# Optimization experiments

Measured on AMD Instinct MI355X. Metric: run time of the kernel, lower is better.

The kernel has to match this reference:

```python
import jax, jax.numpy as jnp
import numpy as np

# Expert output sizes per answer type: yes/no, number, other (VQA v2)
SIZES = [2, 482, 3129]
MAX_ANS = max(SIZES)  # 3129, padded output width
D_IN = 1024
D_HID = 1000
BATCH = 16384
N_TYPES = len(SIZES)


def setup_inputs() -> dict:
    key = jax.random.key(0)
    ks = jax.random.split(key, 2 + 4 * N_TYPES)
    inp = {
        "hidden_states": jax.random.normal(ks[0], (BATCH, D_IN), dtype=jnp.float32),
        "question_type_output": jax.random.normal(ks[1], (BATCH, N_TYPES), dtype=jnp.float32),
    }
    # Learned params for each expert MLP: Linear(1024->1000), Tanh, Linear(1000->n_e)
    for e, n_out in enumerate(SIZES):
        k1, k2, k3, k4 = ks[2 + 4 * e], ks[3 + 4 * e], ks[4 + 4 * e], ks[5 + 4 * e]
        inp[f"w1_{e}"] = jax.random.normal(k1, (D_IN, D_HID), dtype=jnp.float32) * 0.02
        inp[f"b1_{e}"] = jax.random.normal(k2, (D_HID,), dtype=jnp.float32) * 0.02
        inp[f"w2_{e}"] = jax.random.normal(k3, (D_HID, n_out), dtype=jnp.float32) * 0.02
        inp[f"b2_{e}"] = jax.random.normal(k4, (n_out,), dtype=jnp.float32) * 0.02
    return inp


def _expert(x, w1, b1, w2, b2):
    # Linear -> Dropout(eval: identity) -> Tanh -> Linear
    return jnp.tanh(x @ w1 + b1) @ w2 + b2


def reference(hidden_states, question_type_output,
              w1_0, b1_0, w2_0, b2_0,
              w1_1, b1_1, w2_1, b2_1,
              w1_2, b1_2, w2_2, b2_2):
    params = [(w1_0, b1_0, w2_0, b2_0),
              (w1_1, b1_1, w2_1, b2_1),
              (w1_2, b1_2, w2_2, b2_2)]
    # Route each sample to the expert of its argmax question type.
    pred = jnp.argmax(question_type_output, axis=1)  # [B] int
    out = jnp.zeros((hidden_states.shape[0], MAX_ANS), dtype=hidden_states.dtype)
    # Small fixed loop over N_TYPES experts (structurally distinct weights);
    # each expert runs batched over all samples, then a mask selects routed rows.
    for e, (w1, b1, w2, b2) in enumerate(params):
        o = _expert(hidden_states, w1, b1, w2, b2)          # [B, n_e]
        o = jnp.pad(o, ((0, 0), (0, MAX_ANS - o.shape[1])))  # zero-pad to [B, MAX]
        out = jnp.where((pred == e)[:, None], o, out)
    return out
```

## Files before the change

### kernel.cpp

```cpp
#include <hip/hip_runtime.h>

typedef __attribute__((ext_vector_type(8))) __bf16 bf16x8;
typedef __attribute__((ext_vector_type(4))) float f32x4;

constexpr int BATCH = 16384;
constexpr int DIN   = 1024;
constexpr int DHID  = 1000;
constexpr int MAXA  = 3129;
constexpr int MBMAX = 131;

constexpr size_t SZ_AP  = (size_t)MBMAX * 32 * 8192;
constexpr size_t SZ_HP  = SZ_AP;
constexpr size_t SZ_W1P = 3 * 8 * 32 * 8192;
constexpr size_t SZ_W2P = 30 * 32 * 8192;
constexpr size_t WS_HP  = 0;
constexpr size_t WS_W1P = WS_HP + SZ_HP;
constexpr size_t WS_W2P = WS_W1P + SZ_W1P;
constexpr size_t WS_CNT = WS_W2P + SZ_W2P;
constexpr size_t WS_IDX = WS_CNT + 64;
constexpr size_t WS_AP  = WS_IDX + 3 * BATCH * 4;
constexpr size_t WS_NEED = WS_AP + SZ_AP;

constexpr int PA_BLK = 2096;
constexpr int PW1_BLK = 1536;
constexpr int PW2_BLK = 1920;

__device__ __forceinline__ ushort f2bf(float f) {
    return __builtin_bit_cast(ushort, (__bf16)f);
}

__device__ __forceinline__ void gload16(const void* g, void* l) {
    __builtin_amdgcn_global_load_lds((const __attribute__((address_space(1))) void*)g,
                                     (__attribute__((address_space(3))) void*)l, 16, 0, 0);
}

__global__ void route_k(const float* __restrict__ qt, int* __restrict__ counts,
                        int* __restrict__ idx) {
    int i = blockIdx.x * 256 + threadIdx.x;
    if (i >= BATCH) return;
    float a = qt[3 * i], b = qt[3 * i + 1], c = qt[3 * i + 2];
    int p = 0; float m = a;
    if (b > m) { m = b; p = 1; }
    if (c > m) { m = c; p = 2; }
    int pos = atomicAdd(&counts[p], 1);
    idx[p * BATCH + pos] = i;
}

__global__ void pack_all_k(const float* __restrict__ hs,
                           const float* __restrict__ w1_0, const float* __restrict__ w1_1,
                           const float* __restrict__ w1_2,
                           const float* __restrict__ w2_0, const float* __restrict__ w2_1,
                           const float* __restrict__ w2_2,
                           const int* __restrict__ counts, const int* __restrict__ idx,
                           ushort* __restrict__ Ap, ushort* __restrict__ W1p,
                           ushort* __restrict__ W2p) {
    const int b = blockIdx.x, tid = threadIdx.x;
    if (b < PA_BLK) {
        const int g = b * 256 + tid;
        const int m = g & 127, kt = (g >> 7) & 31, mb = g >> 12;
        const int c0 = counts[0], c1 = counts[1], c2 = counts[2];
        const int n0 = (c0 + 127) >> 7, n1 = (c1 + 127) >> 7, n2 = (c2 + 127) >> 7;
        if (mb >= n0 + n1 + n2) return;
        int e = 0, lm = mb, cnt = c0;
        if (lm >= n0) { lm -= n0; e = 1; cnt = c1; }
        if (e == 1 && lm >= n1) { lm -= n1; e = 2; cnt = c2; }
        int ri = lm * 128 + m; if (ri >= cnt) ri = cnt - 1;
        const float* row = hs + (size_t)idx[e * BATCH + ri] * DIN + kt * 32;
        ushort* dst = Ap + (size_t)(mb * 32 + kt) * 4096 + m * 8;
#pragma unroll
        for (int kc = 0; kc < 4; kc++) {
            float4 f0 = *reinterpret_cast<const float4*>(row + kc * 8);
            float4 f1 = *reinterpret_cast<const float4*>(row + kc * 8 + 4);
            union { ushort u[8]; int4 v; } p;
            p.u[0] = f2bf(f0.x); p.u[1] = f2bf(f0.y); p.u[2] = f2bf(f0.z); p.u[3] = f2bf(f0.w);
            p.u[4] = f2bf(f1.x); p.u[5] = f2bf(f1.y); p.u[6] = f2bf(f1.z); p.u[7] = f2bf(f1.w);
            *reinterpret_cast<int4*>(dst + kc * 1024) = p.v;
        }
    } else if (b < PA_BLK + PW1_BLK) {
        const int g = (b - PA_BLK) * 256 + tid;
        const int n = g & 127, kc = (g >> 7) & 3, kt = (g >> 9) & 31, nb = (g >> 14) & 7, e = g >> 17;
        const float* W = e == 0 ? w1_0 : e == 1 ? w1_1 : w1_2;
        const int nn = nb * 128 + n;
        union { ushort u[8]; int4 v; } p;
#pragma unroll
        for (int j = 0; j < 8; j++) {
            int k = kt * 32 + kc * 8 + j;
            float f = (nn < DHID) ? W[(size_t)k * DHID + nn] : 0.f;
            p.u[j] = f2bf(f);
        }
        *reinterpret_cast<int4*>(W1p + ((size_t)((e * 8 + nb) * 32 + kt)) * 4096 + (kc * 128 + n) * 8) = p.v;
    } else {
        const int g = (b - PA_BLK - PW1_BLK) * 256 + tid;
        const int n = g & 127, kc = (g >> 7) & 3, kt = (g >> 9) & 31, t = g >> 14;
        const int e = (t < 1) ? 0 : (t < 5) ? 1 : 2;
        const int nb = t - (e == 0 ? 0 : e == 1 ? 1 : 5);
        const int ne = e == 0 ? 2 : e == 1 ? 482 : MAXA;
        const float* W = e == 0 ? w2_0 : e == 1 ? w2_1 : w2_2;
        const int nn = nb * 128 + n;
        union { ushort u[8]; int4 v; } p;
#pragma unroll
        for (int j = 0; j < 8; j++) {
            int k = kt * 32 + kc * 8 + j;
            float f = (k < DHID && nn < ne) ? W[(size_t)k * ne + nn] : 0.f;
            p.u[j] = f2bf(f);
        }
        *reinterpret_cast<int4*>(W2p + ((size_t)(t * 32 + kt)) * 4096 + (kc * 128 + n) * 8) = p.v;
    }
}

__global__ __launch_bounds__(256, 4)
void gemm1_k(const ushort* __restrict__ Ap, const ushort* __restrict__ W1p,
             const float* __restrict__ b1_0, const float* __restrict__ b1_1,
             const float* __restrict__ b1_2,
             const int* __restrict__ counts, ushort* __restrict__ Hp) {
    const int c0 = counts[0], c1 = counts[1], c2 = counts[2];
    const int n0 = (c0 + 127) >> 7, n1 = (c1 + 127) >> 7, n2 = (c2 + 127) >> 7;
    const int T = (n0 + n1 + n2) * 8;

    const int tid = threadIdx.x;
    const int lane = tid & 63, w = tid >> 6, wm = w >> 1, wn = w & 1;
    const int G = gridDim.x;
    const int v = (blockIdx.x & 7) * (G >> 3) + (blockIdx.x >> 3);

    __shared__ ushort Ab[2][4][128][8];
    __shared__ ushort Bb[2][4][128][8];

    for (int t = v; t < T; t += G) {
        const int mbG = t >> 3, nbk = t & 7;
        int e = 0, lm = mbG;
        if (lm >= n0) { lm -= n0; e = 1; }
        if (e == 1 && lm >= n1) { lm -= n1; e = 2; }
        const float* bias = e == 0 ? b1_0 : e == 1 ? b1_1 : b1_2;
        const char* Atile = (const char*)(Ap + (size_t)mbG * (32 * 4096));
        const char* Btile = (const char*)(W1p + (size_t)((e * 8 + nbk) * 32) * 4096);
        const int soff = w * 2048 + lane * 16;
        char* ad = (char*)&Ab[0][0][0][0] + soff - lane * 16 + lane * 16;

        f32x4 acc[4][4] = {};

        auto stage = [&](int b, int kt) {
            const char* as = Atile + (size_t)kt * 8192 + soff;
            char* adl = (char*)&Ab[b][0][0][0] + w * 2048;
            gload16(as, adl);
            gload16(as + 1024, adl + 1024);
            const char* bs = Btile + (size_t)kt * 8192 + soff;
            char* bdl = (char*)&Bb[b][0][0][0] + w * 2048;
            gload16(bs, bdl);
            gload16(bs + 1024, bdl + 1024);
        };
        auto compute = [&](int b) {
            bf16x8 af[4], bfr[4];
            const int kq = lane >> 4, l15 = lane & 15;
#pragma unroll
            for (int mi = 0; mi < 4; mi++) af[mi] = *reinterpret_cast<const bf16x8*>(&Ab[b][kq][wm * 64 + mi * 16 + l15][0]);
#pragma unroll
            for (int ni = 0; ni < 4; ni++) bfr[ni] = *reinterpret_cast<const bf16x8*>(&Bb[b][kq][wn * 64 + ni * 16 + l15][0]);
#pragma unroll
            for (int mi = 0; mi < 4; mi++)
#pragma unroll
                for (int ni = 0; ni < 4; ni++)
                    acc[mi][ni] = __builtin_amdgcn_mfma_f32_16x16x32_bf16(af[mi], bfr[ni], acc[mi][ni], 0, 0, 0);
        };

        stage(0, 0);
        __syncthreads();
        for (int kt = 0; kt < 32; ++kt) {
            const int cb = kt & 1;
            if (kt + 1 < 32) stage(cb ^ 1, kt + 1);
            compute(cb);
            __syncthreads();
        }

        ushort* Hblk = Hp + (size_t)mbG * (32 * 4096);
#pragma unroll
        for (int mi = 0; mi < 4; mi++) {
            const int mb = wm * 64 + mi * 16 + ((lane >> 4) << 2);
#pragma unroll
            for (int ni = 0; ni < 4; ni++) {
                const int nl = wn * 64 + ni * 16 + (lane & 15);
                const int n = nbk * 128 + nl;
                const bool live = n < DHID;
                const float bv = live ? bias[n] : 0.f;
#pragma unroll
                for (int rg = 0; rg < 4; rg++) {
                    const int m = mb + rg;
                    float vv = live ? tanhf(acc[mi][ni][rg] + bv) : 0.f;
                    Hblk[(size_t)(n >> 5) * 4096 + (((n >> 3) & 3) * 128 + m) * 8 + (n & 7)] = f2bf(vv);
                }
            }
        }
    }
}

__global__ __launch_bounds__(256, 4)
void gemm2_k(const ushort* __restrict__ Hp, const ushort* __restrict__ W2p,
             const float* __restrict__ b2_0, const float* __restrict__ b2_1,
             const float* __restrict__ b2_2,
             const int* __restrict__ counts, const int* __restrict__ idx,
             float* __restrict__ Out) {
    const int c0 = counts[0], c1 = counts[1], c2 = counts[2];
    int nb[3]  = {(c0 + 127) >> 7, (c1 + 127) >> 7, (c2 + 127) >> 7};
    int cc[3]  = {c0, c1, c2};
    const int nbn[3]  = {1, 4, 25};
    const int nz[3]   = {24, 21, 0};
    const int toff[3] = {0, 1, 5};
    const int nel[3]  = {2, 482, MAXA};
    const int Tc = nb[0] * 1 + nb[1] * 4 + nb[2] * 25;
    const int Tz = nb[0] * 24 + nb[1] * 21;
    const int T = Tc + Tz;

    const int tid = threadIdx.x;
    const int lane = tid & 63, w = tid >> 6, wm = w >> 1, wn = w & 1;
    const int G = gridDim.x;
    const int v = (blockIdx.x & 7) * (G >> 3) + (blockIdx.x >> 3);

    __shared__ ushort Ab[2][4][128][8];
    __shared__ ushort Bb[2][4][128][8];

    for (int t = v; t < T; t += G) {
        if (t < Tc) {
            int e = 0, r = t, mbG = 0;
            while (e < 2 && r >= nb[e] * nbn[e]) { r -= nb[e] * nbn[e]; mbG += nb[e]; ++e; }
            const int lm = r / nbn[e], nbk = r - lm * nbn[e];
            mbG += lm;
            const int cnt = cc[e], ne = nel[e];
            const float* bias = e == 0 ? b2_0 : e == 1 ? b2_1 : b2_2;
            const char* Atile = (const char*)(Hp + (size_t)mbG * (32 * 4096));
            const char* Btile = (const char*)(W2p + (size_t)((toff[e] + nbk) * 32) * 4096);
            const int soff = w * 2048 + lane * 16;

            f32x4 acc[4][4] = {};

            auto stage = [&](int b, int kt) {
                const char* as = Atile + (size_t)kt * 8192 + soff;
                char* adl = (char*)&Ab[b][0][0][0] + w * 2048;
                gload16(as, adl);
                gload16(as + 1024, adl + 1024);
                const char* bs = Btile + (size_t)kt * 8192 + soff;
                char* bdl = (char*)&Bb[b][0][0][0] + w * 2048;
                gload16(bs, bdl);
                gload16(bs + 1024, bdl + 1024);
            };
            auto compute = [&](int b) {
                bf16x8 af[4], bfr[4];
                const int kq = lane >> 4, l15 = lane & 15;
#pragma unroll
                for (int mi = 0; mi < 4; mi++) af[mi] = *reinterpret_cast<const bf16x8*>(&Ab[b][kq][wm * 64 + mi * 16 + l15][0]);
#pragma unroll
                for (int ni = 0; ni < 4; ni++) bfr[ni] = *reinterpret_cast<const bf16x8*>(&Bb[b][kq][wn * 64 + ni * 16 + l15][0]);
#pragma unroll
                for (int mi = 0; mi < 4; mi++)
#pragma unroll
                    for (int ni = 0; ni < 4; ni++)
                        acc[mi][ni] = __builtin_amdgcn_mfma_f32_16x16x32_bf16(af[mi], bfr[ni], acc[mi][ni], 0, 0, 0);
            };

            stage(0, 0);
            __syncthreads();
            for (int kt = 0; kt < 32; ++kt) {
                const int cb = kt & 1;
                if (kt + 1 < 32) stage(cb ^ 1, kt + 1);
                compute(cb);
                __syncthreads();
            }

            const int m0 = lm * 128;
#pragma unroll
            for (int mi = 0; mi < 4; mi++) {
                const int mb2 = wm * 64 + mi * 16 + ((lane >> 4) << 2);
#pragma unroll
                for (int ni = 0; ni < 4; ni++) {
                    const int ncol = nbk * 128 + wn * 64 + ni * 16 + (lane & 15);
                    if (ncol >= MAXA) continue;
                    const bool live = ncol < ne;
                    const float bv = live ? bias[ncol] : 0.f;
#pragma unroll
                    for (int rg = 0; rg < 4; rg++) {
                        const int ml = mb2 + rg;
                        if (m0 + ml < cnt) {
                            const int orow = idx[e * BATCH + m0 + ml];
                            Out[(size_t)orow * MAXA + ncol] = live ? (acc[mi][ni][rg] + bv) : 0.f;
                        }
                    }
                }
            }
        } else {
            int e = 0, r = t - Tc;
            while (e < 2 && r >= nb[e] * nz[e]) { r -= nb[e] * nz[e]; ++e; }
            const int lm = r / nz[e], zc = r - lm * nz[e];
            const int cnt = cc[e];
            const int col0 = (e == 0 ? 128 : 512) + zc * 128;
            const int width = (MAXA - col0 < 128) ? (MAXA - col0) : 128;
            const int m0 = lm * 128;
            const int nrow = (cnt - m0 < 128) ? (cnt - m0) : 128;
            const int* rowp = idx + e * BATCH + m0;
            for (int i = tid; i < (nrow << 7); i += 256) {
                const int rl = i >> 7, ccol = i & 127;
                if (ccol < width) Out[(size_t)rowp[rl] * MAXA + col0 + ccol] = 0.f;
            }
        }
    }
}

extern "C" void kernel_launch(void* const* d_in, const int* in_sizes, int n_in,
                              void* d_out, int out_size, void* d_ws, size_t ws_size,
                              hipStream_t stream) {
    const float* hs = (const float*)d_in[0];
    const float* qt = (const float*)d_in[1];
    const float* w1_0 = (const float*)d_in[2],  *b1_0 = (const float*)d_in[3];
    const float* w2_0 = (const float*)d_in[4],  *b2_0 = (const float*)d_in[5];
    const float* w1_1 = (const float*)d_in[6],  *b1_1 = (const float*)d_in[7];
    const float* w2_1 = (const float*)d_in[8],  *b2_1 = (const float*)d_in[9];
    const float* w1_2 = (const float*)d_in[10], *b1_2 = (const float*)d_in[11];
    const float* w2_2 = (const float*)d_in[12], *b2_2 = (const float*)d_in[13];

    char* ws = (char*)d_ws;
    ushort* Hp  = (ushort*)(ws + WS_HP);
    ushort* W1p = (ushort*)(ws + WS_W1P);
    ushort* W2p = (ushort*)(ws + WS_W2P);
    int* counts = (int*)(ws + WS_CNT);
    int* idx    = (int*)(ws + WS_IDX);
    ushort* Ap = (ws_size >= WS_NEED) ? (ushort*)(ws + WS_AP)
               : (ushort*)((char*)d_out + ((size_t)out_size * 4 - SZ_AP));
    float* Out = (float*)d_out;

    hipMemsetAsync(counts, 0, 64, stream);
    route_k<<<64, 256, 0, stream>>>(qt, counts, idx);
    pack_all_k<<<PA_BLK + PW1_BLK + PW2_BLK, 256, 0, stream>>>(
        hs, w1_0, w1_1, w1_2, w2_0, w2_1, w2_2, counts, idx, Ap, W1p, W2p);
    gemm1_k<<<1024, 256, 0, stream>>>(Ap, W1p, b1_0, b1_1, b1_2, counts, Hp);
    gemm2_k<<<1024, 256, 0, stream>>>(Hp, W2p, b2_0, b2_1, b2_2, counts, idx, Out);
}
```

Before: 340.2 us.

## Enlarge GEMM tiles to 256x256 with 512-thread blocks and deep async LDS pipeline

```diff
diff --git a/kernel.cpp b/kernel.cpp
--- a/kernel.cpp
+++ b/kernel.cpp
@@ -7,23 +7,24 @@
 constexpr int DIN   = 1024;
 constexpr int DHID  = 1000;
 constexpr int MAXA  = 3129;
-constexpr int MBMAX = 131;
-
-constexpr size_t SZ_AP  = (size_t)MBMAX * 32 * 8192;
-constexpr size_t SZ_HP  = SZ_AP;
-constexpr size_t SZ_W1P = 3 * 8 * 32 * 8192;
-constexpr size_t SZ_W2P = 30 * 32 * 8192;
+constexpr int MB2   = 66;
+constexpr int KT    = 16;
+
+constexpr size_t TCH    = 32768;
+constexpr size_t SZ_HP  = (size_t)MB2 * KT * TCH;
+constexpr size_t SZ_W1P = (size_t)12 * KT * TCH;
+constexpr size_t SZ_W2P = (size_t)16 * KT * TCH;
 constexpr size_t WS_HP  = 0;
 constexpr size_t WS_W1P = WS_HP + SZ_HP;
 constexpr size_t WS_W2P = WS_W1P + SZ_W1P;
 constexpr size_t WS_CNT = WS_W2P + SZ_W2P;
 constexpr size_t WS_IDX = WS_CNT + 64;
-constexpr size_t WS_AP  = WS_IDX + 3 * BATCH * 4;
-constexpr size_t WS_NEED = WS_AP + SZ_AP;
-
-constexpr int PA_BLK = 2096;
-constexpr int PW1_BLK = 1536;
-constexpr int PW2_BLK = 1920;
+constexpr size_t WS_AP  = WS_IDX + (size_t)3 * BATCH * 4;
+constexpr size_t WS_NEED = WS_AP + SZ_HP;
+
+constexpr int PA_BLK  = MB2 * KT;
+constexpr int PW1_BLK = 12 * KT;
+constexpr int PW2_BLK = 16 * KT;
 
 __device__ __forceinline__ ushort f2bf(float f) {
     return __builtin_bit_cast(ushort, (__bf16)f);
@@ -56,168 +57,194 @@
                            ushort* __restrict__ W2p) {
     const int b = blockIdx.x, tid = threadIdx.x;
     if (b < PA_BLK) {
-        const int g = b * 256 + tid;
-        const int m = g & 127, kt = (g >> 7) & 31, mb = g >> 12;
+        const int mb = b >> 4, kt = b & 15;
         const int c0 = counts[0], c1 = counts[1], c2 = counts[2];
-        const int n0 = (c0 + 127) >> 7, n1 = (c1 + 127) >> 7, n2 = (c2 + 127) >> 7;
+        const int n0 = (c0 + 255) >> 8, n1 = (c1 + 255) >> 8, n2 = (c2 + 255) >> 8;
         if (mb >= n0 + n1 + n2) return;
         int e = 0, lm = mb, cnt = c0;
         if (lm >= n0) { lm -= n0; e = 1; cnt = c1; }
         if (e == 1 && lm >= n1) { lm -= n1; e = 2; cnt = c2; }
-        int ri = lm * 128 + m; if (ri >= cnt) ri = cnt - 1;
-        const float* row = hs + (size_t)idx[e * BATCH + ri] * DIN + kt * 32;
-        ushort* dst = Ap + (size_t)(mb * 32 + kt) * 4096 + m * 8;
-#pragma unroll
-        for (int kc = 0; kc < 4; kc++) {
-            float4 f0 = *reinterpret_cast<const float4*>(row + kc * 8);
-            float4 f1 = *reinterpret_cast<const float4*>(row + kc * 8 + 4);
+        int ri = lm * 256 + tid; if (ri >= cnt) ri = cnt - 1;
+        const float* src = hs + (size_t)idx[e * BATCH + ri] * DIN + kt * 64;
+        ushort* dst = Ap + (size_t)b * 16384 + tid * 8;
+#pragma unroll
+        for (int kq = 0; kq < 8; kq++) {
+            float4 f0 = *reinterpret_cast<const float4*>(src + kq * 8);
+            float4 f1 = *reinterpret_cast<const float4*>(src + kq * 8 + 4);
             union { ushort u[8]; int4 v; } p;
             p.u[0] = f2bf(f0.x); p.u[1] = f2bf(f0.y); p.u[2] = f2bf(f0.z); p.u[3] = f2bf(f0.w);
             p.u[4] = f2bf(f1.x); p.u[5] = f2bf(f1.y); p.u[6] = f2bf(f1.z); p.u[7] = f2bf(f1.w);
-            *reinterpret_cast<int4*>(dst + kc * 1024) = p.v;
+            *reinterpret_cast<int4*>(dst + kq * 2048) = p.v;
         }
     } else if (b < PA_BLK + PW1_BLK) {
-        const int g = (b - PA_BLK) * 256 + tid;
-        const int n = g & 127, kc = (g >> 7) & 3, kt = (g >> 9) & 31, nb = (g >> 14) & 7, e = g >> 17;
+        const int bb = b - PA_BLK;
+        const int kt = bb & 15, nb = (bb >> 4) & 3, e = bb >> 6;
         const float* W = e == 0 ? w1_0 : e == 1 ? w1_1 : w1_2;
-        const int nn = nb * 128 + n;
-        union { ushort u[8]; int4 v; } p;
-#pragma unroll
-        for (int j = 0; j < 8; j++) {
-            int k = kt * 32 + kc * 8 + j;
-            float f = (nn < DHID) ? W[(size_t)k * DHID + nn] : 0.f;
-            p.u[j] = f2bf(f);
-        }
-        *reinterpret_cast<int4*>(W1p + ((size_t)((e * 8 + nb) * 32 + kt)) * 4096 + (kc * 128 + n) * 8) = p.v;
+        const int n = nb * 256 + tid;
+        ushort* dst = W1p + (size_t)bb * 16384 + tid * 8;
+#pragma unroll
+        for (int kq = 0; kq < 8; kq++) {
+            union { ushort u[8]; int4 v; } p;
+#pragma unroll
+            for (int j = 0; j < 8; j++) {
+                int k = kt * 64 + kq * 8 + j;
+                float f = (n < DHID) ? W[(size_t)k * DHID + n] : 0.f;
+                p.u[j] = f2bf(f);
+            }
+            *reinterpret_cast<int4*>(dst + kq * 2048) = p.v;
+        }
     } else {
-        const int g = (b - PA_BLK - PW1_BLK) * 256 + tid;
-        const int n = g & 127, kc = (g >> 7) & 3, kt = (g >> 9) & 31, t = g >> 14;
-        const int e = (t < 1) ? 0 : (t < 5) ? 1 : 2;
-        const int nb = t - (e == 0 ? 0 : e == 1 ? 1 : 5);
+        const int bb = b - PA_BLK - PW1_BLK;
+        const int kt = bb & 15, t = bb >> 4;
+        const int e = (t < 1) ? 0 : (t < 3) ? 1 : 2;
+        const int nb = t - (e == 0 ? 0 : e == 1 ? 1 : 3);
         const int ne = e == 0 ? 2 : e == 1 ? 482 : MAXA;
         const float* W = e == 0 ? w2_0 : e == 1 ? w2_1 : w2_2;
-        const int nn = nb * 128 + n;
-        union { ushort u[8]; int4 v; } p;
-#pragma unroll
-        for (int j = 0; j < 8; j++) {
-            int k = kt * 32 + kc * 8 + j;
-            float f = (k < DHID && nn < ne) ? W[(size_t)k * ne + nn] : 0.f;
-            p.u[j] = f2bf(f);
-        }
-        *reinterpret_cast<int4*>(W2p + ((size_t)(t * 32 + kt)) * 4096 + (kc * 128 + n) * 8) = p.v;
+        const int n = nb * 256 + tid;
+        ushort* dst = W2p + (size_t)bb * 16384 + tid * 8;
+#pragma unroll
+        for (int kq = 0; kq < 8; kq++) {
+            union { ushort u[8]; int4 v; } p;
+#pragma unroll
+            for (int j = 0; j < 8; j++) {
+                int k = kt * 64 + kq * 8 + j;
+                float f = (k < DHID && n < ne) ? W[(size_t)k * ne + n] : 0.f;
+                p.u[j] = f2bf(f);
+            }
+            *reinterpret_cast<int4*>(dst + kq * 2048) = p.v;
+        }
     }
 }
 
-__global__ __launch_bounds__(256, 4)
-void gemm1_k(const ushort* __restrict__ Ap, const ushort* __restrict__ W1p,
+#define PH_BODY(SLOT, KH, MH, LOADB, WAIT, GPH)                                 \
+  {                                                                             \
+    if (WAIT) {                                                                 \
+      asm volatile("s_waitcnt vmcnt(4)" ::: "memory");                          \
+      asm volatile("s_barrier" ::: "memory");                                   \
+    }                                                                           \
+    bf16x8 af[4];                                                               \
+    if (LOADB) {                                                                \
+      _Pragma("unroll")                                                         \
+      for (int ni = 0; ni < 4; ni++)                                            \
+        bfr[ni] = *reinterpret_cast<const bf16x8*>(lds + (SLOT)*65536 + 32768 + \
+                    ((KH)*4 + kq4)*4096 + (wn*64 + ni*16 + l15)*16);            \
+    }                                                                           \
+    _Pragma("unroll")                                                           \
+    for (int mi = 0; mi < 4; mi++)                                              \
+      af[mi] = *reinterpret_cast<const bf16x8*>(lds + (SLOT)*65536 +            \
+                  ((KH)*4 + kq4)*4096 + (wm*128 + (MH)*64 + mi*16 + l15)*16);   \
+    stageh(8*i + (GPH) + 6);                                                    \
+    __builtin_amdgcn_s_setprio(1);                                              \
+    _Pragma("unroll")                                                           \
+    for (int mi = 0; mi < 4; mi++)                                              \
+      _Pragma("unroll")                                                         \
+      for (int ni = 0; ni < 4; ni++)                                            \
+        acc[(MH)*4+mi][ni] = __builtin_amdgcn_mfma_f32_16x16x32_bf16(           \
+            af[mi], bfr[ni], acc[(MH)*4+mi][ni], 0, 0, 0);                      \
+    __builtin_amdgcn_s_setprio(0);                                              \
+    asm volatile("s_barrier" ::: "memory");                                     \
+  }
+
+#define KLOOP(AG, BG)                                                           \
+    asm volatile("s_waitcnt vmcnt(0)" ::: "memory");                            \
+    asm volatile("s_barrier" ::: "memory");                                     \
+    auto stageh = [&](int g) {                                                  \
+        int gw = g & 63;                                                        \
+        int kt2 = gw >> 2, ty = gw & 3;                                         \
+        const char* s = ((ty & 1) ? (BG) : (AG)) + (size_t)kt2 * 32768 +        \
+                        (ty >> 1) * 16384 + tid * 16;                           \
+        char* d = lds + (kt2 & 1) * 65536 + (ty & 1) * 32768 +                  \
+                  (ty >> 1) * 16384 + w * 1024;                                 \
+        gload16(s, d);                                                          \
+        gload16(s + 8192, d + 8192);                                            \
+    };                                                                          \
+    stageh(0); stageh(1); stageh(2); stageh(3); stageh(4); stageh(5);           \
+    f32x4 acc[8][4] = {};                                                       \
+    bf16x8 bfr[4];                                                              \
+    for (int i = 0; i < 8; ++i) {                                               \
+        PH_BODY(0, 0, 0, 1, 1, 0)                                               \
+        PH_BODY(0, 0, 1, 0, 0, 1)                                               \
+        PH_BODY(0, 1, 0, 1, 0, 2)                                               \
+        PH_BODY(0, 1, 1, 0, 0, 3)                                               \
+        PH_BODY(1, 0, 0, 1, 1, 4)                                               \
+        PH_BODY(1, 0, 1, 0, 0, 5)                                               \
+        PH_BODY(1, 1, 0, 1, 0, 6)                                               \
+        PH_BODY(1, 1, 1, 0, 0, 7)                                               \
+    }
+
+__global__ __launch_bounds__(512, 2)
+void gemm1_k(const char* __restrict__ ApB, const char* __restrict__ W1pB,
              const float* __restrict__ b1_0, const float* __restrict__ b1_1,
              const float* __restrict__ b1_2,
              const int* __restrict__ counts, ushort* __restrict__ Hp) {
+    extern __shared__ char lds[];
     const int c0 = counts[0], c1 = counts[1], c2 = counts[2];
-    const int n0 = (c0 + 127) >> 7, n1 = (c1 + 127) >> 7, n2 = (c2 + 127) >> 7;
-    const int T = (n0 + n1 + n2) * 8;
+    const int n0 = (c0 + 255) >> 8, n1 = (c1 + 255) >> 8, n2 = (c2 + 255) >> 8;
+    const int T = (n0 + n1 + n2) * 4;
 
     const int tid = threadIdx.x;
-    const int lane = tid & 63, w = tid >> 6, wm = w >> 1, wn = w & 1;
-    const int G = gridDim.x;
-    const int v = (blockIdx.x & 7) * (G >> 3) + (blockIdx.x >> 3);
-
-    __shared__ ushort Ab[2][4][128][8];
-    __shared__ ushort Bb[2][4][128][8];
-
-    for (int t = v; t < T; t += G) {
-        const int mbG = t >> 3, nbk = t & 7;
+    const int lane = tid & 63, w = tid >> 6;
+    const int wm = w >> 2, wn = w & 3;
+    const int l15 = lane & 15, kq4 = lane >> 4;
+    const int v = (blockIdx.x & 7) * 32 + (blockIdx.x >> 3);
+
+    for (int t = v; t < T; t += 256) {
+        const int mbG = t >> 2, nbk = t & 3;
         int e = 0, lm = mbG;
         if (lm >= n0) { lm -= n0; e = 1; }
         if (e == 1 && lm >= n1) { lm -= n1; e = 2; }
         const float* bias = e == 0 ? b1_0 : e == 1 ? b1_1 : b1_2;
-        const char* Atile = (const char*)(Ap + (size_t)mbG * (32 * 4096));
-        const char* Btile = (const char*)(W1p + (size_t)((e * 8 + nbk) * 32) * 4096);
-        const int soff = w * 2048 + lane * 16;
-        char* ad = (char*)&Ab[0][0][0][0] + soff - lane * 16 + lane * 16;
-
-        f32x4 acc[4][4] = {};
-
-        auto stage = [&](int b, int kt) {
-            const char* as = Atile + (size_t)kt * 8192 + soff;
-            char* adl = (char*)&Ab[b][0][0][0] + w * 2048;
-            gload16(as, adl);
-            gload16(as + 1024, adl + 1024);
-            const char* bs = Btile + (size_t)kt * 8192 + soff;
-            char* bdl = (char*)&Bb[b][0][0][0] + w * 2048;
-            gload16(bs, bdl);
-            gload16(bs + 1024, bdl + 1024);
-        };
-        auto compute = [&](int b) {
-            bf16x8 af[4], bfr[4];
-            const int kq = lane >> 4, l15 = lane & 15;
-#pragma unroll
-            for (int mi = 0; mi < 4; mi++) af[mi] = *reinterpret_cast<const bf16x8*>(&Ab[b][kq][wm * 64 + mi * 16 + l15][0]);
-#pragma unroll
-            for (int ni = 0; ni < 4; ni++) bfr[ni] = *reinterpret_cast<const bf16x8*>(&Bb[b][kq][wn * 64 + ni * 16 + l15][0]);
-#pragma unroll
-            for (int mi = 0; mi < 4; mi++)
-#pragma unroll
-                for (int ni = 0; ni < 4; ni++)
-                    acc[mi][ni] = __builtin_amdgcn_mfma_f32_16x16x32_bf16(af[mi], bfr[ni], acc[mi][ni], 0, 0, 0);
-        };
-
-        stage(0, 0);
-        __syncthreads();
-        for (int kt = 0; kt < 32; ++kt) {
-            const int cb = kt & 1;
-            if (kt + 1 < 32) stage(cb ^ 1, kt + 1);
-            compute(cb);
-            __syncthreads();
-        }
-
-        ushort* Hblk = Hp + (size_t)mbG * (32 * 4096);
-#pragma unroll
-        for (int mi = 0; mi < 4; mi++) {
-            const int mb = wm * 64 + mi * 16 + ((lane >> 4) << 2);
+        const char* Ag = ApB + (size_t)mbG * (KT * TCH);
+        const char* Bg = W1pB + (size_t)((e * 4 + nbk) * KT) * TCH;
+
+        KLOOP(Ag, Bg)
+
+        ushort* Hb = Hp + (size_t)mbG * (KT * 16384);
+#pragma unroll
+        for (int mf = 0; mf < 8; mf++) {
+            const int mr0 = wm * 128 + (mf >> 2) * 64 + (mf & 3) * 16 + kq4 * 4;
 #pragma unroll
             for (int ni = 0; ni < 4; ni++) {
-                const int nl = wn * 64 + ni * 16 + (lane & 15);
-                const int n = nbk * 128 + nl;
+                const int n = nbk * 256 + wn * 64 + ni * 16 + l15;
                 const bool live = n < DHID;
                 const float bv = live ? bias[n] : 0.f;
+                ushort* hb = Hb + (size_t)(n >> 6) * 16384 + ((n >> 3) & 7) * 2048 + (n & 7);
 #pragma unroll
                 for (int rg = 0; rg < 4; rg++) {
-                    const int m = mb + rg;
-                    float vv = live ? tanhf(acc[mi][ni][rg] + bv) : 0.f;
-                    Hblk[(size_t)(n >> 5) * 4096 + (((n >> 3) & 3) * 128 + m) * 8 + (n & 7)] = f2bf(vv);
+                    float vv = live ? tanhf(acc[mf][ni][rg] + bv) : 0.f;
+                    hb[(mr0 + rg) * 8] = f2bf(vv);
                 }
             }
         }
     }
 }
 
-__global__ __launch_bounds__(256, 4)
-void gemm2_k(const ushort* __restrict__ Hp, const ushort* __restrict__ W2p,
+__global__ __launch_bounds__(512, 2)
+void gemm2_k(const char* __restrict__ HpB, const char* __restrict__ W2pB,
              const float* __restrict__ b2_0, const float* __restrict__ b2_1,
              const float* __restrict__ b2_2,
              const int* __restrict__ counts, const int* __restrict__ idx,
              float* __restrict__ Out) {
+    extern __shared__ char lds[];
     const int c0 = counts[0], c1 = counts[1], c2 = counts[2];
-    int nb[3]  = {(c0 + 127) >> 7, (c1 + 127) >> 7, (c2 + 127) >> 7};
+    int nb[3]  = {(c0 + 255) >> 8, (c1 + 255) >> 8, (c2 + 255) >> 8};
     int cc[3]  = {c0, c1, c2};
-    const int nbn[3]  = {1, 4, 25};
-    const int nz[3]   = {24, 21, 0};
-    const int toff[3] = {0, 1, 5};
+    const int nbn[3]  = {1, 2, 13};
+    const int nz[3]   = {12, 11, 0};
+    const int zst[3]  = {256, 512, 0};
+    const int toff[3] = {0, 1, 3};
     const int nel[3]  = {2, 482, MAXA};
-    const int Tc = nb[0] * 1 + nb[1] * 4 + nb[2] * 25;
-    const int Tz = nb[0] * 24 + nb[1] * 21;
+    const int Tc = nb[0] * 1 + nb[1] * 2 + nb[2] * 13;
+    const int Tz = nb[0] * 12 + nb[1] * 11;
     const int T = Tc + Tz;
 
     const int tid = threadIdx.x;
-    const int lane = tid & 63, w = tid >> 6, wm = w >> 1, wn = w & 1;
-    const int G = gridDim.x;
-    const int v = (blockIdx.x & 7) * (G >> 3) + (blockIdx.x >> 3);
-
-    __shared__ ushort Ab[2][4][128][8];
-    __shared__ ushort Bb[2][4][128][8];
-
-    for (int t = v; t < T; t += G) {
+    const int lane = tid & 63, w = tid >> 6;
+    const int wm = w >> 2, wn = w & 3;
+    const int l15 = lane & 15, kq4 = lane >> 4;
+    const int v = (blockIdx.x & 7) * 32 + (blockIdx.x >> 3);
+
+    for (int t = v; t < T; t += 256) {
         if (t < Tc) {
             int e = 0, r = t, mbG = 0;
             while (e < 2 && r >= nb[e] * nbn[e]) { r -= nb[e] * nbn[e]; mbG += nb[e]; ++e; }
@@ -225,61 +252,28 @@
             mbG += lm;
             const int cnt = cc[e], ne = nel[e];
             const float* bias = e == 0 ? b2_0 : e == 1 ? b2_1 : b2_2;
-            const char* Atile = (const char*)(Hp + (size_t)mbG * (32 * 4096));
-            const char* Btile = (const char*)(W2p + (size_t)((toff[e] + nbk) * 32) * 4096);
-            const int soff = w * 2048 + lane * 16;
-
-            f32x4 acc[4][4] = {};
-
-            auto stage = [&](int b, int kt) {
-                const char* as = Atile + (size_t)kt * 8192 + soff;
-                char* adl = (char*)&Ab[b][0][0][0] + w * 2048;
-                gload16(as, adl);
-                gload16(as + 1024, adl + 1024);
-                const char* bs = Btile + (size_t)kt * 8192 + soff;
-                char* bdl = (char*)&Bb[b][0][0][0] + w * 2048;
-                gload16(bs, bdl);
-                gload16(bs + 1024, bdl + 1024);
-            };
-            auto compute = [&](int b) {
-                bf16x8 af[4], bfr[4];
-                const int kq = lane >> 4, l15 = lane & 15;
-#pragma unroll
-                for (int mi = 0; mi < 4; mi++) af[mi] = *reinterpret_cast<const bf16x8*>(&Ab[b][kq][wm * 64 + mi * 16 + l15][0]);
-#pragma unroll
-                for (int ni = 0; ni < 4; ni++) bfr[ni] = *reinterpret_cast<const bf16x8*>(&Bb[b][kq][wn * 64 + ni * 16 + l15][0]);
-#pragma unroll
-                for (int mi = 0; mi < 4; mi++)
-#pragma unroll
-                    for (int ni = 0; ni < 4; ni++)
-                        acc[mi][ni] = __builtin_amdgcn_mfma_f32_16x16x32_bf16(af[mi], bfr[ni], acc[mi][ni], 0, 0, 0);
-            };
-
-            stage(0, 0);
-            __syncthreads();
-            for (int kt = 0; kt < 32; ++kt) {
-                const int cb = kt & 1;
-                if (kt + 1 < 32) stage(cb ^ 1, kt + 1);
-                compute(cb);
-                __syncthreads();
-            }
-
-            const int m0 = lm * 128;
-#pragma unroll
-            for (int mi = 0; mi < 4; mi++) {
-                const int mb2 = wm * 64 + mi * 16 + ((lane >> 4) << 2);
+            const char* Ag = HpB + (size_t)mbG * (KT * TCH);
+            const char* Bg = W2pB + (size_t)((toff[e] + nbk) * KT) * TCH;
+
+            KLOOP(Ag, Bg)
+
+            const int m0 = lm * 256;
+            const int* ip = idx + e * BATCH + m0;
+#pragma unroll
+            for (int mf = 0; mf < 8; mf++) {
+                const int mr0 = wm * 128 + (mf >> 2) * 64 + (mf & 3) * 16 + kq4 * 4;
 #pragma unroll
                 for (int ni = 0; ni < 4; ni++) {
-                    const int ncol = nbk * 128 + wn * 64 + ni * 16 + (lane & 15);
+                    const int ncol = nbk * 256 + wn * 64 + ni * 16 + l15;
                     if (ncol >= MAXA) continue;
                     const bool live = ncol < ne;
                     const float bv = live ? bias[ncol] : 0.f;
 #pragma unroll
                     for (int rg = 0; rg < 4; rg++) {
-                        const int ml = mb2 + rg;
-                        if (m0 + ml < cnt) {
-                            const int orow = idx[e * BATCH + m0 + ml];
-                            Out[(size_t)orow * MAXA + ncol] = live ? (acc[mi][ni][rg] + bv) : 0.f;
+                        const int m = mr0 + rg;
+                        if (m0 + m < cnt) {
+                            const int orow = ip[m];
+                            Out[(size_t)orow * MAXA + ncol] = live ? (acc[mf][ni][rg] + bv) : 0.f;
                         }
                     }
                 }
@@ -289,14 +283,15 @@
             while (e < 2 && r >= nb[e] * nz[e]) { r -= nb[e] * nz[e]; ++e; }
             const int lm = r / nz[e], zc = r - lm * nz[e];
             const int cnt = cc[e];
-            const int col0 = (e == 0 ? 128 : 512) + zc * 128;
-            const int width = (MAXA - col0 < 128) ? (MAXA - col0) : 128;
-            const int m0 = lm * 128;
-            const int nrow = (cnt - m0 < 128) ? (cnt - m0) : 128;
+            const int col0 = zst[e] + zc * 256;
+            const int width = (MAXA - col0 < 256) ? (MAXA - col0) : 256;
+            const int m0 = lm * 256;
+            const int nrow = (cnt - m0 < 256) ? (cnt - m0) : 256;
             const int* rowp = idx + e * BATCH + m0;
-            for (int i = tid; i < (nrow << 7); i += 256) {
-                const int rl = i >> 7, ccol = i & 127;
-                if (ccol < width) Out[(size_t)rowp[rl] * MAXA + col0 + ccol] = 0.f;
+            const int tot = nrow * width;
+            for (int i2 = tid; i2 < tot; i2 += 512) {
+                const int rl = i2 / width, ccol = i2 - rl * width;
+                Out[(size_t)rowp[rl] * MAXA + col0 + ccol] = 0.f;
             }
         }
     }
@@ -321,13 +316,15 @@
     int* counts = (int*)(ws + WS_CNT);
     int* idx    = (int*)(ws + WS_IDX);
     ushort* Ap = (ws_size >= WS_NEED) ? (ushort*)(ws + WS_AP)
-               : (ushort*)((char*)d_out + ((size_t)out_size * 4 - SZ_AP));
+               : (ushort*)((char*)d_out + ((size_t)out_size * 4 - SZ_HP));
     float* Out = (float*)d_out;
 
     hipMemsetAsync(counts, 0, 64, stream);
     route_k<<<64, 256, 0, stream>>>(qt, counts, idx);
     pack_all_k<<<PA_BLK + PW1_BLK + PW2_BLK, 256, 0, stream>>>(
         hs, w1_0, w1_1, w1_2, w2_0, w2_1, w2_2, counts, idx, Ap, W1p, W2p);
-    gemm1_k<<<1024, 256, 0, stream>>>(Ap, W1p, b1_0, b1_1, b1_2, counts, Hp);
-    gemm2_k<<<1024, 256, 0, stream>>>(Hp, W2p, b2_0, b2_1, b2_2, counts, idx, Out);
-}
+    gemm1_k<<<256, 512, 131072, stream>>>((const char*)Ap, (const char*)W1p,
+                                          b1_0, b1_1, b1_2, counts, Hp);
+    gemm2_k<<<256, 512, 131072, stream>>>((const char*)Hp, (const char*)W2p,
+                                          b2_0, b2_1, b2_2, counts, idx, Out);
+}
```

New measurement: 394.0 us. 15.8% more time.

## Triple-buffer GEMM K-loop and stage epilogues through LDS for coalesced stores

Applied to the files above, without the earlier changes.

```diff
diff --git a/kernel.cpp b/kernel.cpp
--- a/kernel.cpp
+++ b/kernel.cpp
@@ -108,101 +108,127 @@
     }
 }
 
-__global__ __launch_bounds__(256, 4)
-void gemm1_k(const ushort* __restrict__ Ap, const ushort* __restrict__ W1p,
+#define STAGE(BUFO, KT)                                                         \
+    {                                                                           \
+        const char* as_ = Ag + (size_t)(KT) * 8192 + tid * 16;                  \
+        char* ad_ = lds + (BUFO) + w * 1024;                                    \
+        gload16(as_, ad_);                                                      \
+        gload16(as_ + 4096, ad_ + 4096);                                        \
+        const char* bs_ = Bg + (size_t)(KT) * 8192 + tid * 16;                  \
+        gload16(bs_, ad_ + 8192);                                               \
+        gload16(bs_ + 4096, ad_ + 12288);                                       \
+    }
+
+#define KLOOP()                                                                 \
+    f32x4 acc[4][4] = {};                                                       \
+    STAGE(0, 0)                                                                 \
+    STAGE(16384, 1)                                                             \
+    {                                                                           \
+        int cur = 0;                                                            \
+        for (int kt = 0; kt < 32; ++kt) {                                       \
+            if (kt < 31) asm volatile("s_waitcnt vmcnt(4)" ::: "memory");       \
+            else         asm volatile("s_waitcnt vmcnt(0)" ::: "memory");       \
+            asm volatile("s_barrier" ::: "memory");                             \
+            if (kt + 2 < 32) {                                                  \
+                int nx = cur + 2; if (nx >= 3) nx -= 3;                         \
+                STAGE(nx * 16384, kt + 2)                                       \
+            }                                                                   \
+            const char* base = lds + cur * 16384;                               \
+            bf16x8 af[4], bfr[4];                                               \
+            _Pragma("unroll")                                                   \
+            for (int mi = 0; mi < 4; mi++)                                      \
+                af[mi] = *reinterpret_cast<const bf16x8*>(                      \
+                    base + kq4 * 2048 + (wm * 64 + mi * 16 + l15) * 16);        \
+            _Pragma("unroll")                                                   \
+            for (int ni = 0; ni < 4; ni++)                                      \
+                bfr[ni] = *reinterpret_cast<const bf16x8*>(                     \
+                    base + 8192 + kq4 * 2048 + (wn * 64 + ni * 16 + l15) * 16); \
+            __builtin_amdgcn_s_setprio(1);                                      \
+            _Pragma("unroll")                                                   \
+            for (int mi = 0; mi < 4; mi++)                                      \
+                _Pragma("unroll")                                               \
+                for (int ni = 0; ni < 4; ni++)                                  \
+                    acc[mi][ni] = __builtin_amdgcn_mfma_f32_16x16x32_bf16(      \
+                        af[mi], bfr[ni], acc[mi][ni], 0, 0, 0);                 \
+            __builtin_amdgcn_s_setprio(0);                                      \
+            cur = cur + 1; if (cur == 3) cur = 0;                               \
+        }                                                                       \
+    }                                                                           \
+    asm volatile("s_barrier" ::: "memory");
+
+__global__ __launch_bounds__(256, 3)
+void gemm1_k(const char* __restrict__ ApB, const char* __restrict__ W1pB,
              const float* __restrict__ b1_0, const float* __restrict__ b1_1,
              const float* __restrict__ b1_2,
-             const int* __restrict__ counts, ushort* __restrict__ Hp) {
+             const int* __restrict__ counts, char* __restrict__ HpB) {
+    __shared__ __align__(16) char lds[49152];
     const int c0 = counts[0], c1 = counts[1], c2 = counts[2];
     const int n0 = (c0 + 127) >> 7, n1 = (c1 + 127) >> 7, n2 = (c2 + 127) >> 7;
     const int T = (n0 + n1 + n2) * 8;
 
     const int tid = threadIdx.x;
     const int lane = tid & 63, w = tid >> 6, wm = w >> 1, wn = w & 1;
-    const int G = gridDim.x;
-    const int v = (blockIdx.x & 7) * (G >> 3) + (blockIdx.x >> 3);
-
-    __shared__ ushort Ab[2][4][128][8];
-    __shared__ ushort Bb[2][4][128][8];
-
-    for (int t = v; t < T; t += G) {
+    const int l15 = lane & 15, kq4 = lane >> 4;
+    const int v = (blockIdx.x & 7) * 96 + (blockIdx.x >> 3);
+
+    for (int t = v; t < T; t += 768) {
         const int mbG = t >> 3, nbk = t & 7;
         int e = 0, lm = mbG;
         if (lm >= n0) { lm -= n0; e = 1; }
         if (e == 1 && lm >= n1) { lm -= n1; e = 2; }
         const float* bias = e == 0 ? b1_0 : e == 1 ? b1_1 : b1_2;
-        const char* Atile = (const char*)(Ap + (size_t)mbG * (32 * 4096));
-        const char* Btile = (const char*)(W1p + (size_t)((e * 8 + nbk) * 32) * 4096);
-        const int soff = w * 2048 + lane * 16;
-        char* ad = (char*)&Ab[0][0][0][0] + soff - lane * 16 + lane * 16;
-
-        f32x4 acc[4][4] = {};
-
-        auto stage = [&](int b, int kt) {
-            const char* as = Atile + (size_t)kt * 8192 + soff;
-            char* adl = (char*)&Ab[b][0][0][0] + w * 2048;
-            gload16(as, adl);
-            gload16(as + 1024, adl + 1024);
-            const char* bs = Btile + (size_t)kt * 8192 + soff;
-            char* bdl = (char*)&Bb[b][0][0][0] + w * 2048;
-            gload16(bs, bdl);
-            gload16(bs + 1024, bdl + 1024);
-        };
-        auto compute = [&](int b) {
-            bf16x8 af[4], bfr[4];
-            const int kq = lane >> 4, l15 = lane & 15;
-#pragma unroll
-            for (int mi = 0; mi < 4; mi++) af[mi] = *reinterpret_cast<const bf16x8*>(&Ab[b][kq][wm * 64 + mi * 16 + l15][0]);
-#pragma unroll
-            for (int ni = 0; ni < 4; ni++) bfr[ni] = *reinterpret_cast<const bf16x8*>(&Bb[b][kq][wn * 64 + ni * 16 + l15][0]);
-#pragma unroll
-            for (int mi = 0; mi < 4; mi++)
-#pragma unroll
-                for (int ni = 0; ni < 4; ni++)
-                    acc[mi][ni] = __builtin_amdgcn_mfma_f32_16x16x32_bf16(af[mi], bfr[ni], acc[mi][ni], 0, 0, 0);
-        };
-
-        stage(0, 0);
-        __syncthreads();
-        for (int kt = 0; kt < 32; ++kt) {
-            const int cb = kt & 1;
-            if (kt + 1 < 32) stage(cb ^ 1, kt + 1);
-            compute(cb);
-            __syncthreads();
-        }
-
-        ushort* Hblk = Hp + (size_t)mbG * (32 * 4096);
+        const char* Ag = ApB + (size_t)mbG * (32 * 8192);
+        const char* Bg = W1pB + (size_t)((e * 8 + nbk) * 32) * 8192;
+
+        KLOOP()
+
+        ushort* img = (ushort*)lds;
 #pragma unroll
         for (int mi = 0; mi < 4; mi++) {
-            const int mb = wm * 64 + mi * 16 + ((lane >> 4) << 2);
+            const int rb = wm * 64 + mi * 16 + kq4 * 4;
 #pragma unroll
             for (int ni = 0; ni < 4; ni++) {
-                const int nl = wn * 64 + ni * 16 + (lane & 15);
-                const int n = nbk * 128 + nl;
-                const bool live = n < DHID;
-                const float bv = live ? bias[n] : 0.f;
+                const int nl = wn * 64 + ni * 16 + l15;
+                const int ng = nbk * 128 + nl;
+                const bool live = ng < DHID;
+                const float bv = live ? bias[ng] : 0.f;
+                const int ua = ((nl >> 5) * 4096 + ((nl >> 3) & 3) * 1024 + (nl & 6)) & ~1;
 #pragma unroll
                 for (int rg = 0; rg < 4; rg++) {
-                    const int m = mb + rg;
                     float vv = live ? tanhf(acc[mi][ni][rg] + bv) : 0.f;
-                    Hblk[(size_t)(n >> 5) * 4096 + (((n >> 3) & 3) * 128 + m) * 8 + (n & 7)] = f2bf(vv);
+                    float vo = __shfl_xor(vv, 1);
+                    ushort lo = (l15 & 1) ? f2bf(vo) : f2bf(vv);
+                    ushort hi = (l15 & 1) ? f2bf(vv) : f2bf(vo);
+                    *reinterpret_cast<uint*>(img + ua + (rb + rg) * 8) =
+                        (uint)lo | ((uint)hi << 16);
                 }
             }
         }
+        asm volatile("s_barrier" ::: "memory");
+        char* hdst = HpB + ((size_t)mbG * 32 + nbk * 4) * 8192;
+#pragma unroll
+        for (int i2 = 0; i2 < 8; i2++) {
+            const int s = tid + i2 * 256;
+            *reinterpret_cast<int4*>(hdst + s * 16) =
+                *reinterpret_cast<const int4*>(lds + s * 16);
+        }
+        asm volatile("s_barrier" ::: "memory");
     }
 }
 
-__global__ __launch_bounds__(256, 4)
-void gemm2_k(const ushort* __restrict__ Hp, const ushort* __restrict__ W2p,
+__global__ __launch_bounds__(256, 3)
+void gemm2_k(const char* __restrict__ HpB, const char* __restrict__ W2pB,
              const float* __restrict__ b2_0, const float* __restrict__ b2_1,
              const float* __restrict__ b2_2,
              const int* __restrict__ counts, const int* __restrict__ idx,
              float* __restrict__ Out) {
+    __shared__ __align__(16) char lds[49152];
     const int c0 = counts[0], c1 = counts[1], c2 = counts[2];
     int nb[3]  = {(c0 + 127) >> 7, (c1 + 127) >> 7, (c2 + 127) >> 7};
     int cc[3]  = {c0, c1, c2};
     const int nbn[3]  = {1, 4, 25};
     const int nz[3]   = {24, 21, 0};
+    const int zst[3]  = {128, 512, 0};
     const int toff[3] = {0, 1, 5};
     const int nel[3]  = {2, 482, MAXA};
     const int Tc = nb[0] * 1 + nb[1] * 4 + nb[2] * 25;
@@ -211,13 +237,10 @@
 
     const int tid = threadIdx.x;
     const int lane = tid & 63, w = tid >> 6, wm = w >> 1, wn = w & 1;
-    const int G = gridDim.x;
-    const int v = (blockIdx.x & 7) * (G >> 3) + (blockIdx.x >> 3);
-
-    __shared__ ushort Ab[2][4][128][8];
-    __shared__ ushort Bb[2][4][128][8];
-
-    for (int t = v; t < T; t += G) {
+    const int l15 = lane & 15, kq4 = lane >> 4;
+    const int v = (blockIdx.x & 7) * 96 + (blockIdx.x >> 3);
+
+    for (int t = v; t < T; t += 768) {
         if (t < Tc) {
             int e = 0, r = t, mbG = 0;
             while (e < 2 && r >= nb[e] * nbn[e]) { r -= nb[e] * nbn[e]; mbG += nb[e]; ++e; }
@@ -225,78 +248,83 @@
             mbG += lm;
             const int cnt = cc[e], ne = nel[e];
             const float* bias = e == 0 ? b2_0 : e == 1 ? b2_1 : b2_2;
-            const char* Atile = (const char*)(Hp + (size_t)mbG * (32 * 4096));
-            const char* Btile = (const char*)(W2p + (size_t)((toff[e] + nbk) * 32) * 4096);
-            const int soff = w * 2048 + lane * 16;
-
-            f32x4 acc[4][4] = {};
-
-            auto stage = [&](int b, int kt) {
-                const char* as = Atile + (size_t)kt * 8192 + soff;
-                char* adl = (char*)&Ab[b][0][0][0] + w * 2048;
-                gload16(as, adl);
-                gload16(as + 1024, adl + 1024);
-                const char* bs = Btile + (size_t)kt * 8192 + soff;
-                char* bdl = (char*)&Bb[b][0][0][0] + w * 2048;
-                gload16(bs, bdl);
-                gload16(bs + 1024, bdl + 1024);
-            };
-            auto compute = [&](int b) {
-                bf16x8 af[4], bfr[4];
-                const int kq = lane >> 4, l15 = lane & 15;
-#pragma unroll
-                for (int mi = 0; mi < 4; mi++) af[mi] = *reinterpret_cast<const bf16x8*>(&Ab[b][kq][wm * 64 + mi * 16 + l15][0]);
-#pragma unroll
-                for (int ni = 0; ni < 4; ni++) bfr[ni] = *reinterpret_cast<const bf16x8*>(&Bb[b][kq][wn * 64 + ni * 16 + l15][0]);
-#pragma unroll
-                for (int mi = 0; mi < 4; mi++)
-#pragma unroll
-                    for (int ni = 0; ni < 4; ni++)
-                        acc[mi][ni] = __builtin_amdgcn_mfma_f32_16x16x32_bf16(af[mi], bfr[ni], acc[mi][ni], 0, 0, 0);
-            };
-
-            stage(0, 0);
-            __syncthreads();
-            for (int kt = 0; kt < 32; ++kt) {
-                const int cb = kt & 1;
-                if (kt + 1 < 32) stage(cb ^ 1, kt + 1);
-                compute(cb);
-                __syncthreads();
-            }
+            const char* Ag = HpB + (size_t)mbG * (32 * 8192);
+            const char* Bg = W2pB + (size_t)((toff[e] + nbk) * 32) * 8192;
+
+            KLOOP()
 
             const int m0 = lm * 128;
-#pragma unroll
-            for (int mi = 0; mi < 4; mi++) {
-                const int mb2 = wm * 64 + mi * 16 + ((lane >> 4) << 2);
-#pragma unroll
-                for (int ni = 0; ni < 4; ni++) {
-                    const int ncol = nbk * 128 + wn * 64 + ni * 16 + (lane & 15);
-                    if (ncol >= MAXA) continue;
-                    const bool live = ncol < ne;
-                    const float bv = live ? bias[ncol] : 0.f;
-#pragma unroll
-                    for (int rg = 0; rg < 4; rg++) {
-                        const int ml = mb2 + rg;
-                        if (m0 + ml < cnt) {
-                            const int orow = idx[e * BATCH + m0 + ml];
-                            Out[(size_t)orow * MAXA + ncol] = live ? (acc[mi][ni][rg] + bv) : 0.f;
+            float* bf32 = (float*)lds;
+            const int* ip = idx + e * BATCH;
+#pragma unroll
+            for (int h = 0; h < 2; h++) {
+                if (wm == h) {
+#pragma unroll
+                    for (int mi = 0; mi < 4; mi++) {
+                        const int rl = mi * 16 + kq4 * 4;
+#pragma unroll
+                        for (int ni = 0; ni < 4; ni++) {
+                            const int nl = wn * 64 + ni * 16 + l15;
+                            const int ncol = nbk * 128 + nl;
+                            const bool live = ncol < ne;
+                            const float bv = live ? bias[ncol] : 0.f;
+#pragma unroll
+                            for (int rg = 0; rg < 4; rg++)
+                                bf32[(rl + rg) * 132 + nl] =
+                                    live ? (acc[mi][ni][rg] + bv) : 0.f;
                         }
                     }
                 }
+                asm volatile("s_barrier" ::: "memory");
+#pragma unroll
+                for (int i2 = 0; i2 < 8; i2++) {
+                    const int s = tid + i2 * 256;
+                    const int rr = s >> 5, c4 = s & 31;
+                    const int mrow = m0 + h * 64 + rr;
+                    if (mrow < cnt) {
+                        const int orow = ip[mrow];
+                        const int ncol0 = nbk * 128 + c4 * 4;
+                        float4 val = *reinterpret_cast<const float4*>(bf32 + rr * 132 + c4 * 4);
+                        float* op = Out + (size_t)orow * MAXA + ncol0;
+                        if (ncol0 + 3 < MAXA) {
+                            *reinterpret_cast<float4*>(op) = val;
+                        } else {
+                            if (ncol0 + 0 < MAXA) op[0] = val.x;
+                            if (ncol0 + 1 < MAXA) op[1] = val.y;
+                            if (ncol0 + 2 < MAXA) op[2] = val.z;
+                            if (ncol0 + 3 < MAXA) op[3] = val.w;
+                        }
+                    }
+                }
+                asm volatile("s_barrier" ::: "memory");
             }
         } else {
             int e = 0, r = t - Tc;
             while (e < 2 && r >= nb[e] * nz[e]) { r -= nb[e] * nz[e]; ++e; }
             const int lm = r / nz[e], zc = r - lm * nz[e];
             const int cnt = cc[e];
-            const int col0 = (e == 0 ? 128 : 512) + zc * 128;
+            const int col0 = zst[e] + zc * 128;
             const int width = (MAXA - col0 < 128) ? (MAXA - col0) : 128;
             const int m0 = lm * 128;
             const int nrow = (cnt - m0 < 128) ? (cnt - m0) : 128;
             const int* rowp = idx + e * BATCH + m0;
-            for (int i = tid; i < (nrow << 7); i += 256) {
-                const int rl = i >> 7, ccol = i & 127;
-                if (ccol < width) Out[(size_t)rowp[rl] * MAXA + col0 + ccol] = 0.f;
+            const float4 z4 = {0.f, 0.f, 0.f, 0.f};
+            if (width == 128) {
+                for (int s = tid; s < (nrow << 5); s += 256) {
+                    const int rl = s >> 5, c4 = s & 31;
+                    *reinterpret_cast<float4*>(Out + (size_t)rowp[rl] * MAXA + col0 + c4 * 4) = z4;
+                }
+            } else {
+                const int f4 = width >> 2;
+                for (int s = tid; s < nrow * f4; s += 256) {
+                    const int rl = s / f4, c4 = s - rl * f4;
+                    *reinterpret_cast<float4*>(Out + (size_t)rowp[rl] * MAXA + col0 + c4 * 4) = z4;
+                }
+                const int rem = width & 3;
+                for (int s = tid; s < nrow * rem; s += 256) {
+                    const int rl = s / rem, j = s - rl * rem;
+                    Out[(size_t)rowp[rl] * MAXA + col0 + f4 * 4 + j] = 0.f;
+                }
             }
         }
     }
@@ -328,6 +356,8 @@
     route_k<<<64, 256, 0, stream>>>(qt, counts, idx);
     pack_all_k<<<PA_BLK + PW1_BLK + PW2_BLK, 256, 0, stream>>>(
         hs, w1_0, w1_1, w1_2, w2_0, w2_1, w2_2, counts, idx, Ap, W1p, W2p);
-    gemm1_k<<<1024, 256, 0, stream>>>(Ap, W1p, b1_0, b1_1, b1_2, counts, Hp);
-    gemm2_k<<<1024, 256, 0, stream>>>(Hp, W2p, b2_0, b2_1, b2_2, counts, idx, Out);
-}
+    gemm1_k<<<768, 256, 0, stream>>>((const char*)Ap, (const char*)W1p,
+                                     b1_0, b1_1, b1_2, counts, (char*)Hp);
+    gemm2_k<<<768, 256, 0, stream>>>((const char*)Hp, (const char*)W2p,
+                                     b2_0, b2_1, b2_2, counts, idx, Out);
+}
```

After: 318.1 us. 6.5% less time.
